# Kernel tuning notes

Hardware: AMD Instinct MI355X
Metric: run time of the kernel (lower is better)

## Reference

```python
import jax, jax.numpy as jnp
import numpy as np

HIDDEN = 1024
HEADS = 16
HEAD_DIM = HIDDEN // HEADS  # 64
B, S = 2, 2048


def setup_inputs() -> dict:
    key = jax.random.key(0)
    ks = jax.random.split(key, 12)
    lim_h = 1.0 / np.sqrt(HEAD_DIM)
    lim_o = 1.0 / np.sqrt(HIDDEN)
    u = lambda k, shape, lim: jax.random.uniform(k, shape, jnp.float32, -lim, lim)
    return {
        "query": jax.random.normal(ks[0], (B, S, HIDDEN), jnp.float32),
        "key": jax.random.normal(ks[1], (B, S, HIDDEN), jnp.float32),
        "value": jax.random.normal(ks[2], (B, S, HIDDEN), jnp.float32),
        "mask": jax.random.randint(ks[3], (B, 1, S, S), 0, 2, jnp.int32),
        "Wq": u(ks[4], (HEAD_DIM, HEAD_DIM), lim_h), "bq": u(ks[5], (HEAD_DIM,), lim_h),
        "Wk": u(ks[6], (HEAD_DIM, HEAD_DIM), lim_h), "bk": u(ks[7], (HEAD_DIM,), lim_h),
        "Wv": u(ks[8], (HEAD_DIM, HEAD_DIM), lim_h), "bv": u(ks[9], (HEAD_DIM,), lim_h),
        "Wo": u(ks[10], (HIDDEN, HIDDEN), lim_o), "bo": u(ks[11], (HIDDEN,), lim_o),
    }


def reference(query, key, value, mask, Wq, bq, Wk, bk, Wv, bv, Wo, bo):
    b = query.shape[0]
    # view [B, S, H, D]; per-head linear is SHARED across heads (head_dim x head_dim)
    q = query.reshape(b, -1, HEADS, HEAD_DIM) @ Wq.T + bq
    k = key.reshape(b, -1, HEADS, HEAD_DIM) @ Wk.T + bk
    v = value.reshape(b, -1, HEADS, HEAD_DIM) @ Wv.T + bv
    scores = jnp.einsum('nqhd,nkhd->nhqk', q, k)  # [B, H, Sq, Sk]
    scores = jnp.where(mask == 0, jnp.float32(-1e20), scores)
    # NOTE: original scales by sqrt(hidden_dim), not sqrt(head_dim)
    attn = jax.nn.softmax(scores / np.sqrt(HIDDEN).astype(np.float32), axis=3)
    out = jnp.einsum('nhql,nlhd->nqhd', attn, v).reshape(b, query.shape[1], HIDDEN)
    return out @ Wo.T + bo
```

## Files before the change

### kernel.cpp

```cpp
#include <hip/hip_runtime.h>
#include <hip/hip_bf16.h>

#define NB 2
#define NS 2048
#define NH 16
#define ND 64
#define NHID 1024

#define QSCALE 0.045084220f

typedef __attribute__((ext_vector_type(8))) short bf16x8;
typedef __attribute__((ext_vector_type(4))) short s16x4;
typedef __attribute__((ext_vector_type(4))) float f32x4;

typedef __attribute__((address_space(3))) unsigned int lds_u32;
typedef __attribute__((address_space(1))) unsigned int glb_u32;

__device__ inline void gl_lds16(const void* g, void* l) {
  __builtin_amdgcn_global_load_lds((const glb_u32*)g, (lds_u32*)l, 16, 0, 0);
}

__device__ inline short f2bf(float f) {
  __hip_bfloat16 h = __float2bfloat16(f);
  short s; __builtin_memcpy(&s, &h, 2); return s;
}

__device__ inline unsigned pk2bf(float a, float b) {
  float2 t; t.x = a; t.y = b;
  __hip_bfloat162 h = __float22bfloat162_rn(t);
  unsigned u; __builtin_memcpy(&u, &h, 4); return u;
}

__device__ inline bf16x8 cvt8(const float* __restrict__ p) {
  float4 x = *(const float4*)p;
  float4 y = *(const float4*)(p + 4);
  bf16x8 r;
  r[0] = f2bf(x.x); r[1] = f2bf(x.y); r[2] = f2bf(x.z); r[3] = f2bf(x.w);
  r[4] = f2bf(y.x); r[5] = f2bf(y.y); r[6] = f2bf(y.z); r[7] = f2bf(y.w);
  return r;
}

__global__ __launch_bounds__(256) void prep(
    const int* __restrict__ mask, unsigned* __restrict__ mp,
    const float* __restrict__ Wq, const float* __restrict__ Wk,
    const float* __restrict__ Wv, const float* __restrict__ Wo,
    short* __restrict__ Wq_b, short* __restrict__ Wk_b,
    short* __restrict__ Wv_b, short* __restrict__ Wo_b)
{
  if (blockIdx.x < 1024) {
    int idx = blockIdx.x * 256 + threadIdx.x;
    const int4* src = (const int4*)(mask + (long)idx * 32);
    unsigned w = 0;
#pragma unroll
    for (int i = 0; i < 8; ++i) {
      int4 v = src[i];
      w |= (v.x != 0 ? 1u : 0u) << (i * 4 + 0);
      w |= (v.y != 0 ? 1u : 0u) << (i * 4 + 1);
      w |= (v.z != 0 ? 1u : 0u) << (i * 4 + 2);
      w |= (v.w != 0 ? 1u : 0u) << (i * 4 + 3);
    }
    mp[idx] = w;
  } else {
    int i = ((blockIdx.x - 1024) * 256 + threadIdx.x) * 4;
    const float* src; short* dst; int off; float sc = 1.0f;
    if (i < 1048576)      { src = Wo; dst = Wo_b; off = i; }
    else {
      int j = i - 1048576;
      if (j < 4096)       { src = Wq; dst = Wq_b; off = j; sc = QSCALE; }
      else if (j < 8192)  { src = Wk; dst = Wk_b; off = j - 4096; }
      else                { src = Wv; dst = Wv_b; off = j - 8192; }
    }
    float4 v = *(const float4*)(src + off);
    s16x4 o;
    o[0] = f2bf(v.x * sc); o[1] = f2bf(v.y * sc);
    o[2] = f2bf(v.z * sc); o[3] = f2bf(v.w * sc);
    *(s16x4*)(dst + off) = o;
  }
}

__global__ __launch_bounds__(256) void qkv_proj(
    const float* __restrict__ qin, const float* __restrict__ kin,
    const float* __restrict__ vin,
    const short* __restrict__ Wq_b, const float* __restrict__ bq,
    const short* __restrict__ Wk_b, const float* __restrict__ bk,
    const short* __restrict__ Wv_b, const float* __restrict__ bv,
    short* __restrict__ Qws, short* __restrict__ Kws, short* __restrict__ Vt)
{
  __shared__ __align__(16) short ldsT[4][16][72];
  __shared__ __align__(16) short ldsVT[64][72];
  const int tid = threadIdx.x;
  const int w = tid >> 6, lane = tid & 63;
  const int c = lane & 15, qq = lane >> 4;

  if (blockIdx.x < 1024) {
    const int t = blockIdx.x * 4 + w;
    const int b = t >> 11, s = t & (NS - 1);
    const int aoff = (t * 16 + c) * 64 + qq * 8;
    const int row0 = lane >> 3, inner = lane & 7;

#pragma unroll
    for (int m = 0; m < 2; ++m) {
      const float* X  = (m == 0) ? qin  : kin;
      const short* W  = (m == 0) ? Wq_b : Wk_b;
      const float* bb = (m == 0) ? bq   : bk;
      short* dst      = (m == 0) ? Qws  : Kws;
      const float bsc = (m == 0) ? QSCALE : 1.0f;

      bf16x8 a0 = cvt8(X + aoff);
      bf16x8 a1 = cvt8(X + aoff + 32);

#pragma unroll
      for (int nt = 0; nt < 4; ++nt) {
        f32x4 z = {0.f, 0.f, 0.f, 0.f};
        const short* wp = W + (nt * 16 + c) * 64 + qq * 8;
        bf16x8 b0 = *(const bf16x8*)(wp);
        bf16x8 b1 = *(const bf16x8*)(wp + 32);
        z = __builtin_amdgcn_mfma_f32_16x16x32_bf16(a0, b0, z, 0, 0, 0);
        z = __builtin_amdgcn_mfma_f32_16x16x32_bf16(a1, b1, z, 0, 0, 0);
        float bias = bb[nt * 16 + c] * bsc;
#pragma unroll
        for (int r = 0; r < 4; ++r)
          ldsT[w][qq * 4 + r][nt * 16 + c] = f2bf(z[r] + bias);
      }

      bf16x8 v0 = *(const bf16x8*)&ldsT[w][row0][inner * 8];
      bf16x8 v1 = *(const bf16x8*)&ldsT[w][row0 + 8][inner * 8];
      int bh0 = b * NH + row0, bh1 = b * NH + row0 + 8;
      *(bf16x8*)(dst + (bh0 * NS + s) * 64 + inner * 8) = v0;
      *(bf16x8*)(dst + (bh1 * NS + s) * 64 + inner * 8) = v1;
    }
  } else {
    const int bid = blockIdx.x - 1024;
    const int g = w;
    const int bh = bid >> 5;
    const int stile = bid & 31;
    const int b = bh >> 4, h = bh & 15;
    const int sb = stile * 64;

    bf16x8 wv[8];
    float bias[4];
#pragma unroll
    for (int nt = 0; nt < 4; ++nt) {
      const short* wp = Wv_b + (nt * 16 + c) * 64 + qq * 8;
      wv[nt * 2]     = *(const bf16x8*)(wp);
      wv[nt * 2 + 1] = *(const bf16x8*)(wp + 32);
      bias[nt] = bv[nt * 16 + c];
    }

    const float* ap = vin + ((size_t)((b * NS + sb + 16 * g + c) * 16 + h)) * 64 + qq * 8;
    bf16x8 a0 = cvt8(ap);
    bf16x8 a1 = cvt8(ap + 32);
#pragma unroll
    for (int nt = 0; nt < 4; ++nt) {
      f32x4 z = {0.f, 0.f, 0.f, 0.f};
      z = __builtin_amdgcn_mfma_f32_16x16x32_bf16(a0, wv[nt * 2], z, 0, 0, 0);
      z = __builtin_amdgcn_mfma_f32_16x16x32_bf16(a1, wv[nt * 2 + 1], z, 0, 0, 0);
      uint2 u;
      u.x = pk2bf(z[0] + bias[nt], z[1] + bias[nt]);
      u.y = pk2bf(z[2] + bias[nt], z[3] + bias[nt]);
      *(uint2*)&ldsVT[nt * 16 + c][16 * g + qq * 4] = u;
    }
    __syncthreads();

#pragma unroll
    for (int j = 0; j < 2; ++j) {
      int idx = tid + 256 * j;
      int d = idx >> 3, unit = idx & 7;
      bf16x8 o = *(const bf16x8*)&ldsVT[d][unit * 8];
      *(bf16x8*)(Vt + ((size_t)(bh * 64 + d)) * NS + sb + unit * 8) = o;
    }
  }
}

__global__ __launch_bounds__(256) void attn(
    const short* __restrict__ Qws, const short* __restrict__ Kws,
    const short* __restrict__ Vt, const unsigned* __restrict__ Mp,
    short* __restrict__ AO)
{
  __shared__ __align__(16) short Ks[2][64][64];
  __shared__ __align__(16) short Vs[2][64][64];
  __shared__ __align__(16) short Ps[4][32][72];

  const int tid = threadIdx.x;
  const int w = tid >> 6, lane = tid & 63;
  const int c = lane & 15, qq = lane >> 4;
  const int bh = blockIdx.x & 31;
  const int qtile = blockIdx.x >> 5;
  const int b = bh >> 4, h = bh & 15;
  const int qbase = qtile * 128 + w * 32;

  const short* Qp = Qws + (size_t)bh * (NS * 64);
  const short* Kp = Kws + (size_t)bh * (NS * 64);
  const short* Vp = Vt + (size_t)bh * (64 * NS);
  const unsigned* mrow = Mp + (size_t)b * (NS * (NS / 32));

  bf16x8 aq[2][2];
#pragma unroll
  for (int nq = 0; nq < 2; ++nq) {
    const short* qp = Qp + (qbase + nq * 16 + c) * 64 + qq * 8;
    aq[nq][0] = *(const bf16x8*)(qp);
    aq[nq][1] = *(const bf16x8*)(qp + 32);
  }

  bf16x8 ones;
#pragma unroll
  for (int i = 0; i < 8; ++i) ones[i] = (short)0x3F80;

  const f32x4 ZV = {0.f, 0.f, 0.f, 0.f};
  f32x4 O[2][4];
  f32x4 Osum[2];
#pragma unroll
  for (int nq = 0; nq < 2; ++nq) {
    Osum[nq] = ZV;
#pragma unroll
    for (int dt = 0; dt < 4; ++dt) O[nq][dt] = ZV;
  }

  const int srow = lane >> 3;
  const int sunit = (lane & 7) ^ srow;
  auto stage = [&](int kt, int buf) {
#pragma unroll
    for (int i = 0; i < 2; ++i) {
      int j = w * 2 + i;
      const short* gk = Kp + ((size_t)(kt * 64 + j * 8 + srow)) * 64 + sunit * 8;
      gl_lds16(gk, &Ks[buf][0][0] + j * 512);
      const short* gv = Vp + ((size_t)(j * 8 + srow)) * NS + kt * 64 + sunit * 8;
      gl_lds16(gv, &Vs[buf][0][0] + j * 512);
    }
  };

  stage(0, 0);
  __syncthreads();

  for (int kt = 0; kt < NS / 64; ++kt) {
    const int buf = kt & 1;
    if (kt < NS / 64 - 1) stage(kt + 1, buf ^ 1);

    uint2 mw[2];
#pragma unroll
    for (int nq = 0; nq < 2; ++nq)
      mw[nq] = *(const uint2*)(mrow +
          (size_t)(qbase + nq * 16 + c) * (NS / 32) + kt * 2);

#pragma unroll
    for (int mt = 0; mt < 4; ++mt) {
      const short* kb = &Ks[buf][mt * 16 + c][0];
      bf16x8 ak0 = *(const bf16x8*)(kb + ((qq ^ (c & 7)) << 3));
      bf16x8 ak1 = *(const bf16x8*)(kb + (((4 + qq) ^ (c & 7)) << 3));
#pragma unroll
      for (int nq = 0; nq < 2; ++nq) {
        f32x4 z = __builtin_amdgcn_mfma_f32_16x16x32_bf16(ak0, aq[nq][0], ZV, 0, 0, 0);
        z = __builtin_amdgcn_mfma_f32_16x16x32_bf16(ak1, aq[nq][1], z, 0, 0, 0);
        unsigned wsel = (mt & 2) ? mw[nq].y : mw[nq].x;
        unsigned nib = (wsel >> (((mt & 1) << 4) + (qq << 2))) & 0xFu;
        float e0 = __builtin_amdgcn_exp2f((nib & 1u) ? z[0] : -128.f);
        float e1 = __builtin_amdgcn_exp2f((nib & 2u) ? z[1] : -128.f);
        float e2 = __builtin_amdgcn_exp2f((nib & 4u) ? z[2] : -128.f);
        float e3 = __builtin_amdgcn_exp2f((nib & 8u) ? z[3] : -128.f);
        uint2 u;
        u.x = pk2bf(e0, e1);
        u.y = pk2bf(e2, e3);
        *(uint2*)&Ps[w][nq * 16 + c][mt * 16 + (qq << 2)] = u;
      }
    }

#pragma unroll
    for (int ks = 0; ks < 2; ++ks) {
      bf16x8 pf[2];
#pragma unroll
      for (int nq = 0; nq < 2; ++nq) {
        pf[nq] = *(const bf16x8*)&Ps[w][nq * 16 + c][ks * 32 + qq * 8];
        Osum[nq] = __builtin_amdgcn_mfma_f32_16x16x32_bf16(ones, pf[nq], Osum[nq], 0, 0, 0);
      }
#pragma unroll
      for (int dt = 0; dt < 4; ++dt) {
        const short* vb = &Vs[buf][dt * 16 + c][0];
        bf16x8 vf = *(const bf16x8*)(vb + ((((ks << 2) + qq) ^ (c & 7)) << 3));
#pragma unroll
        for (int nq = 0; nq < 2; ++nq)
          O[nq][dt] = __builtin_amdgcn_mfma_f32_16x16x32_bf16(vf, pf[nq], O[nq][dt], 0, 0, 0);
      }
    }

    __syncthreads();
  }

#pragma unroll
  for (int nq = 0; nq < 2; ++nq) {
    float inv = 1.0f / fmaxf(Osum[nq][0], 1e-30f);
    int row = qbase + nq * 16 + c;
#pragma unroll
    for (int dt = 0; dt < 4; ++dt) {
      uint2 u;
      u.x = pk2bf(O[nq][dt][0] * inv, O[nq][dt][1] * inv);
      u.y = pk2bf(O[nq][dt][2] * inv, O[nq][dt][3] * inv);
      *(uint2*)(AO + ((size_t)(b * NS + row)) * NHID + h * 64 + dt * 16 + qq * 4) = u;
    }
  }
}

__global__ __launch_bounds__(256, 2) void oproj(
    const short* __restrict__ X, const short* __restrict__ Wo_b,
    const float* __restrict__ bo, float* __restrict__ out)
{
  __shared__ __align__(16) short As[2][64][64];
  __shared__ __align__(16) short Bs[2][128][64];
  const int tid = threadIdx.x;
  const int w = tid >> 6, lane = tid & 63;
  const int c = lane & 15, qq = lane >> 4;
  const int rowbase = blockIdx.x * 64;
  const int colbase = blockIdx.y * 128;
  const int mh = w & 1, nh = w >> 1;

  const int srow = lane >> 3;
  const int sunit = (lane & 7) ^ srow;

  auto stage = [&](int kb, int buf) {
#pragma unroll
    for (int i = 0; i < 6; ++i) {
      int t = w * 6 + i;
      if (t < 8) {
        const short* g = X + (size_t)(rowbase + t * 8 + srow) * NHID
                           + kb * 64 + sunit * 8;
        gl_lds16(g, &As[buf][0][0] + t * 512);
      } else {
        int j = t - 8;
        const short* g = Wo_b + (size_t)(colbase + j * 8 + srow) * NHID
                              + kb * 64 + sunit * 8;
        gl_lds16(g, &Bs[buf][0][0] + j * 512);
      }
    }
  };

  f32x4 acc[2][4];
#pragma unroll
  for (int mt = 0; mt < 2; ++mt)
#pragma unroll
    for (int nt = 0; nt < 4; ++nt) { f32x4 z = {0.f, 0.f, 0.f, 0.f}; acc[mt][nt] = z; }

  stage(0, 0);
  __syncthreads();

  for (int kb = 0; kb < NHID / 64; ++kb) {
    const int buf = kb & 1;
    if (kb < NHID / 64 - 1) stage(kb + 1, buf ^ 1);

    bf16x8 af[2][2];
#pragma unroll
    for (int mt = 0; mt < 2; ++mt) {
      const short* ap = &As[buf][mh * 32 + mt * 16 + c][0];
#pragma unroll
      for (int ks = 0; ks < 2; ++ks)
        af[mt][ks] = *(const bf16x8*)(ap + ((((ks << 2) + qq) ^ (c & 7)) << 3));
    }
#pragma unroll
    for (int nt = 0; nt < 4; ++nt) {
      const short* bp = &Bs[buf][nh * 64 + nt * 16 + c][0];
#pragma unroll
      for (int ks = 0; ks < 2; ++ks) {
        bf16x8 bf = *(const bf16x8*)(bp + ((((ks << 2) + qq) ^ (c & 7)) << 3));
#pragma unroll
        for (int mt = 0; mt < 2; ++mt)
          acc[mt][nt] = __builtin_amdgcn_mfma_f32_16x16x32_bf16(af[mt][ks], bf, acc[mt][nt], 0, 0, 0);
      }
    }

    __syncthreads();
  }

#pragma unroll
  for (int nt = 0; nt < 4; ++nt) {
    int col = colbase + nh * 64 + nt * 16 + c;
    float bias = bo[col];
#pragma unroll
    for (int mt = 0; mt < 2; ++mt) {
      int row = rowbase + mh * 32 + mt * 16 + qq * 4;
#pragma unroll
      for (int r = 0; r < 4; ++r)
        out[(size_t)(row + r) * NHID + col] = acc[mt][nt][r] + bias;
    }
  }
}

extern "C" void kernel_launch(void* const* d_in, const int* in_sizes, int n_in,
                              void* d_out, int out_size, void* d_ws, size_t ws_size,
                              hipStream_t stream) {
  const float* qin = (const float*)d_in[0];
  const float* kin = (const float*)d_in[1];
  const float* vin = (const float*)d_in[2];
  const int*  mask = (const int*)d_in[3];
  const float* Wq = (const float*)d_in[4];
  const float* bq = (const float*)d_in[5];
  const float* Wk = (const float*)d_in[6];
  const float* bk = (const float*)d_in[7];
  const float* Wv = (const float*)d_in[8];
  const float* bv = (const float*)d_in[9];
  const float* Wo = (const float*)d_in[10];
  const float* bo = (const float*)d_in[11];
  float* out = (float*)d_out;

  char* ws = (char*)d_ws;
  short* Qws = (short*)(ws);
  short* Kws = (short*)(ws + (size_t)(8 << 20));
  short* Vt  = (short*)(ws + (size_t)(16 << 20));
  short* AO  = (short*)(ws + (size_t)(24 << 20));
  unsigned* Mp = (unsigned*)(ws + (size_t)(32 << 20));
  short* Wo_b = (short*)(ws + (size_t)(33 << 20));
  short* Wq_b = (short*)(ws + (size_t)(35 << 20));
  short* Wk_b = (short*)(ws + (size_t)(35 << 20) + 8192);
  short* Wv_b = (short*)(ws + (size_t)(35 << 20) + 16384);

  prep<<<2060, 256, 0, stream>>>(mask, Mp, Wq, Wk, Wv, Wo, Wq_b, Wk_b, Wv_b, Wo_b);
  qkv_proj<<<2048, 256, 0, stream>>>(qin, kin, vin, Wq_b, bq, Wk_b, bk, Wv_b, bv,
                                     Qws, Kws, Vt);
  attn<<<(NB * NH) * (NS / 128), 256, 0, stream>>>(Qws, Kws, Vt, Mp, AO);
  oproj<<<dim3(64, 8), 256, 0, stream>>>(AO, Wo_b, bo, out);
}
```

Baseline: 222.5 us.

## Load V fragments directly from global, replace MFMA row-sum with scalar sum

The attention kernel stops staging V tiles through LDS and instead has each lane load its V MFMA fragments straight from global memory into registers at the top of each key tile. The softmax denominator is now accumulated as a per-lane fp32 sum of the exponentials and reduced with cross-lane shuffles at the end, replacing the extra MFMA against a ones vector. Launch bounds now request four blocks per CU. This cuts LDS traffic and footprint and removes MFMA work, but exposes global-load latency for V with only the loop-level prefetch of K overlapping it, and raises register pressure from holding eight V fragments.

```diff
diff --git a/kernel.cpp b/kernel.cpp
--- a/kernel.cpp
+++ b/kernel.cpp
@@ -172,13 +172,12 @@
   }
 }
 
-__global__ __launch_bounds__(256) void attn(
+__global__ __launch_bounds__(256, 4) void attn(
     const short* __restrict__ Qws, const short* __restrict__ Kws,
     const short* __restrict__ Vt, const unsigned* __restrict__ Mp,
     short* __restrict__ AO)
 {
   __shared__ __align__(16) short Ks[2][64][64];
-  __shared__ __align__(16) short Vs[2][64][64];
   __shared__ __align__(16) short Ps[4][32][72];
 
   const int tid = threadIdx.x;
@@ -202,39 +201,41 @@
     aq[nq][1] = *(const bf16x8*)(qp + 32);
   }
 
-  bf16x8 ones;
-#pragma unroll
-  for (int i = 0; i < 8; ++i) ones[i] = (short)0x3F80;
-
   const f32x4 ZV = {0.f, 0.f, 0.f, 0.f};
+  float lsum[2] = {0.f, 0.f};
   f32x4 O[2][4];
-  f32x4 Osum[2];
-#pragma unroll
-  for (int nq = 0; nq < 2; ++nq) {
-    Osum[nq] = ZV;
+#pragma unroll
+  for (int nq = 0; nq < 2; ++nq)
 #pragma unroll
     for (int dt = 0; dt < 4; ++dt) O[nq][dt] = ZV;
-  }
 
   const int srow = lane >> 3;
   const int sunit = (lane & 7) ^ srow;
-  auto stage = [&](int kt, int buf) {
+  auto stageK = [&](int kt, int buf) {
 #pragma unroll
     for (int i = 0; i < 2; ++i) {
       int j = w * 2 + i;
       const short* gk = Kp + ((size_t)(kt * 64 + j * 8 + srow)) * 64 + sunit * 8;
       gl_lds16(gk, &Ks[buf][0][0] + j * 512);
-      const short* gv = Vp + ((size_t)(j * 8 + srow)) * NS + kt * 64 + sunit * 8;
-      gl_lds16(gv, &Vs[buf][0][0] + j * 512);
     }
   };
 
-  stage(0, 0);
+  stageK(0, 0);
   __syncthreads();
 
   for (int kt = 0; kt < NS / 64; ++kt) {
     const int buf = kt & 1;
-    if (kt < NS / 64 - 1) stage(kt + 1, buf ^ 1);
+    const int kbase = kt * 64;
+
+    bf16x8 vf[8];
+#pragma unroll
+    for (int ks = 0; ks < 2; ++ks)
+#pragma unroll
+      for (int dt = 0; dt < 4; ++dt)
+        vf[ks * 4 + dt] = *(const bf16x8*)(Vp +
+            (size_t)(dt * 16 + c) * NS + kbase + ks * 32 + qq * 8);
+
+    if (kt < NS / 64 - 1) stageK(kt + 1, buf ^ 1);
 
     uint2 mw[2];
 #pragma unroll
@@ -257,6 +258,7 @@
         float e1 = __builtin_amdgcn_exp2f((nib & 2u) ? z[1] : -128.f);
         float e2 = __builtin_amdgcn_exp2f((nib & 4u) ? z[2] : -128.f);
         float e3 = __builtin_amdgcn_exp2f((nib & 8u) ? z[3] : -128.f);
+        lsum[nq] += (e0 + e1) + (e2 + e3);
         uint2 u;
         u.x = pk2bf(e0, e1);
         u.y = pk2bf(e2, e3);
@@ -268,18 +270,13 @@
     for (int ks = 0; ks < 2; ++ks) {
       bf16x8 pf[2];
 #pragma unroll
-      for (int nq = 0; nq < 2; ++nq) {
+      for (int nq = 0; nq < 2; ++nq)
         pf[nq] = *(const bf16x8*)&Ps[w][nq * 16 + c][ks * 32 + qq * 8];
-        Osum[nq] = __builtin_amdgcn_mfma_f32_16x16x32_bf16(ones, pf[nq], Osum[nq], 0, 0, 0);
-      }
-#pragma unroll
-      for (int dt = 0; dt < 4; ++dt) {
-        const short* vb = &Vs[buf][dt * 16 + c][0];
-        bf16x8 vf = *(const bf16x8*)(vb + ((((ks << 2) + qq) ^ (c & 7)) << 3));
+#pragma unroll
+      for (int dt = 0; dt < 4; ++dt)
 #pragma unroll
         for (int nq = 0; nq < 2; ++nq)
-          O[nq][dt] = __builtin_amdgcn_mfma_f32_16x16x32_bf16(vf, pf[nq], O[nq][dt], 0, 0, 0);
-      }
+          O[nq][dt] = __builtin_amdgcn_mfma_f32_16x16x32_bf16(vf[ks * 4 + dt], pf[nq], O[nq][dt], 0, 0, 0);
     }
 
     __syncthreads();
@@ -287,13 +284,20 @@
 
 #pragma unroll
   for (int nq = 0; nq < 2; ++nq) {
-    float inv = 1.0f / fmaxf(Osum[nq][0], 1e-30f);
+    float v = lsum[nq];
+    v += __shfl_xor(v, 16);
+    v += __shfl_xor(v, 32);
+    lsum[nq] = 1.0f / fmaxf(v, 1e-30f);
+  }
+
+#pragma unroll
+  for (int nq = 0; nq < 2; ++nq) {
     int row = qbase + nq * 16 + c;
 #pragma unroll
     for (int dt = 0; dt < 4; ++dt) {
       uint2 u;
-      u.x = pk2bf(O[nq][dt][0] * inv, O[nq][dt][1] * inv);
-      u.y = pk2bf(O[nq][dt][2] * inv, O[nq][dt][3] * inv);
+      u.x = pk2bf(O[nq][dt][0] * lsum[nq], O[nq][dt][1] * lsum[nq]);
+      u.y = pk2bf(O[nq][dt][2] * lsum[nq], O[nq][dt][3] * lsum[nq]);
       *(uint2*)(AO + ((size_t)(b * NS + row)) * NHID + h * 64 + dt * 16 + qq * 4) = u;
     }
   }
```

Result: slower. 260.5 us (+17.0%).

## Fuse prep into projection kernel and replace MFMA row-sum with scalar sums

Applied to the files above, without the earlier changes.

Merges the mask-packing and weight-conversion prep kernel into the QKV projection kernel as extra block ranges. The small Wq/Wk/Wv weights are now converted to bf16 on the fly inside each block instead of being staged through workspace. This removes one launch and the dependency between the two kernels, at the cost of redundant per-block weight conversion. In attention, the softmax denominator is now accumulated from the fp32 exponentials with cross-lane shuffles rather than an extra ones-vector MFMA per tile, which cuts matrix-core work and uses unrounded values for the sum.

```diff
diff --git a/kernel.cpp b/kernel.cpp
--- a/kernel.cpp
+++ b/kernel.cpp
@@ -34,57 +34,30 @@
 __device__ inline bf16x8 cvt8(const float* __restrict__ p) {
   float4 x = *(const float4*)p;
   float4 y = *(const float4*)(p + 4);
-  bf16x8 r;
-  r[0] = f2bf(x.x); r[1] = f2bf(x.y); r[2] = f2bf(x.z); r[3] = f2bf(x.w);
-  r[4] = f2bf(y.x); r[5] = f2bf(y.y); r[6] = f2bf(y.z); r[7] = f2bf(y.w);
-  return r;
-}
-
-__global__ __launch_bounds__(256) void prep(
-    const int* __restrict__ mask, unsigned* __restrict__ mp,
-    const float* __restrict__ Wq, const float* __restrict__ Wk,
-    const float* __restrict__ Wv, const float* __restrict__ Wo,
-    short* __restrict__ Wq_b, short* __restrict__ Wk_b,
-    short* __restrict__ Wv_b, short* __restrict__ Wo_b)
-{
-  if (blockIdx.x < 1024) {
-    int idx = blockIdx.x * 256 + threadIdx.x;
-    const int4* src = (const int4*)(mask + (long)idx * 32);
-    unsigned w = 0;
-#pragma unroll
-    for (int i = 0; i < 8; ++i) {
-      int4 v = src[i];
-      w |= (v.x != 0 ? 1u : 0u) << (i * 4 + 0);
-      w |= (v.y != 0 ? 1u : 0u) << (i * 4 + 1);
-      w |= (v.z != 0 ? 1u : 0u) << (i * 4 + 2);
-      w |= (v.w != 0 ? 1u : 0u) << (i * 4 + 3);
-    }
-    mp[idx] = w;
-  } else {
-    int i = ((blockIdx.x - 1024) * 256 + threadIdx.x) * 4;
-    const float* src; short* dst; int off; float sc = 1.0f;
-    if (i < 1048576)      { src = Wo; dst = Wo_b; off = i; }
-    else {
-      int j = i - 1048576;
-      if (j < 4096)       { src = Wq; dst = Wq_b; off = j; sc = QSCALE; }
-      else if (j < 8192)  { src = Wk; dst = Wk_b; off = j - 4096; }
-      else                { src = Wv; dst = Wv_b; off = j - 8192; }
-    }
-    float4 v = *(const float4*)(src + off);
-    s16x4 o;
-    o[0] = f2bf(v.x * sc); o[1] = f2bf(v.y * sc);
-    o[2] = f2bf(v.z * sc); o[3] = f2bf(v.w * sc);
-    *(s16x4*)(dst + off) = o;
-  }
-}
-
-__global__ __launch_bounds__(256) void qkv_proj(
+  unsigned u[4];
+  u[0] = pk2bf(x.x, x.y); u[1] = pk2bf(x.z, x.w);
+  u[2] = pk2bf(y.x, y.y); u[3] = pk2bf(y.z, y.w);
+  bf16x8 r; __builtin_memcpy(&r, u, 16); return r;
+}
+
+__device__ inline bf16x8 cvt8s(const float* __restrict__ p, float sc) {
+  float4 x = *(const float4*)p;
+  float4 y = *(const float4*)(p + 4);
+  unsigned u[4];
+  u[0] = pk2bf(x.x * sc, x.y * sc); u[1] = pk2bf(x.z * sc, x.w * sc);
+  u[2] = pk2bf(y.x * sc, y.y * sc); u[3] = pk2bf(y.z * sc, y.w * sc);
+  bf16x8 r; __builtin_memcpy(&r, u, 16); return r;
+}
+
+__global__ __launch_bounds__(256) void fused_front(
     const float* __restrict__ qin, const float* __restrict__ kin,
-    const float* __restrict__ vin,
-    const short* __restrict__ Wq_b, const float* __restrict__ bq,
-    const short* __restrict__ Wk_b, const float* __restrict__ bk,
-    const short* __restrict__ Wv_b, const float* __restrict__ bv,
-    short* __restrict__ Qws, short* __restrict__ Kws, short* __restrict__ Vt)
+    const float* __restrict__ vin, const int* __restrict__ mask,
+    const float* __restrict__ Wq, const float* __restrict__ bq,
+    const float* __restrict__ Wk, const float* __restrict__ bk,
+    const float* __restrict__ Wv, const float* __restrict__ bv,
+    const float* __restrict__ Wo,
+    short* __restrict__ Qws, short* __restrict__ Kws, short* __restrict__ Vt,
+    unsigned* __restrict__ mp, short* __restrict__ Wo_b)
 {
   __shared__ __align__(16) short ldsT[4][16][72];
   __shared__ __align__(16) short ldsVT[64][72];
@@ -100,24 +73,24 @@
 
 #pragma unroll
     for (int m = 0; m < 2; ++m) {
-      const float* X  = (m == 0) ? qin  : kin;
-      const short* W  = (m == 0) ? Wq_b : Wk_b;
-      const float* bb = (m == 0) ? bq   : bk;
-      short* dst      = (m == 0) ? Qws  : Kws;
-      const float bsc = (m == 0) ? QSCALE : 1.0f;
+      const float* X  = (m == 0) ? qin : kin;
+      const float* Wf = (m == 0) ? Wq  : Wk;
+      const float* bb = (m == 0) ? bq  : bk;
+      short* dst      = (m == 0) ? Qws : Kws;
+      const float sc  = (m == 0) ? QSCALE : 1.0f;
 
       bf16x8 a0 = cvt8(X + aoff);
       bf16x8 a1 = cvt8(X + aoff + 32);
 
 #pragma unroll
       for (int nt = 0; nt < 4; ++nt) {
+        const float* wp = Wf + (nt * 16 + c) * 64 + qq * 8;
+        bf16x8 b0 = cvt8s(wp, sc);
+        bf16x8 b1 = cvt8s(wp + 32, sc);
         f32x4 z = {0.f, 0.f, 0.f, 0.f};
-        const short* wp = W + (nt * 16 + c) * 64 + qq * 8;
-        bf16x8 b0 = *(const bf16x8*)(wp);
-        bf16x8 b1 = *(const bf16x8*)(wp + 32);
         z = __builtin_amdgcn_mfma_f32_16x16x32_bf16(a0, b0, z, 0, 0, 0);
         z = __builtin_amdgcn_mfma_f32_16x16x32_bf16(a1, b1, z, 0, 0, 0);
-        float bias = bb[nt * 16 + c] * bsc;
+        float bias = bb[nt * 16 + c] * sc;
 #pragma unroll
         for (int r = 0; r < 4; ++r)
           ldsT[w][qq * 4 + r][nt * 16 + c] = f2bf(z[r] + bias);
@@ -129,7 +102,7 @@
       *(bf16x8*)(dst + (bh0 * NS + s) * 64 + inner * 8) = v0;
       *(bf16x8*)(dst + (bh1 * NS + s) * 64 + inner * 8) = v1;
     }
-  } else {
+  } else if (blockIdx.x < 2048) {
     const int bid = blockIdx.x - 1024;
     const int g = w;
     const int bh = bid >> 5;
@@ -141,9 +114,9 @@
     float bias[4];
 #pragma unroll
     for (int nt = 0; nt < 4; ++nt) {
-      const short* wp = Wv_b + (nt * 16 + c) * 64 + qq * 8;
-      wv[nt * 2]     = *(const bf16x8*)(wp);
-      wv[nt * 2 + 1] = *(const bf16x8*)(wp + 32);
+      const float* wp = Wv + (nt * 16 + c) * 64 + qq * 8;
+      wv[nt * 2]     = cvt8(wp);
+      wv[nt * 2 + 1] = cvt8(wp + 32);
       bias[nt] = bv[nt * 16 + c];
     }
 
@@ -169,6 +142,26 @@
       bf16x8 o = *(const bf16x8*)&ldsVT[d][unit * 8];
       *(bf16x8*)(Vt + ((size_t)(bh * 64 + d)) * NS + sb + unit * 8) = o;
     }
+  } else if (blockIdx.x < 3072) {
+    int idx = (blockIdx.x - 2048) * 256 + tid;
+    const int4* src = (const int4*)(mask + (long)idx * 32);
+    unsigned wbits = 0;
+#pragma unroll
+    for (int i = 0; i < 8; ++i) {
+      int4 v = src[i];
+      wbits |= (v.x != 0 ? 1u : 0u) << (i * 4 + 0);
+      wbits |= (v.y != 0 ? 1u : 0u) << (i * 4 + 1);
+      wbits |= (v.z != 0 ? 1u : 0u) << (i * 4 + 2);
+      wbits |= (v.w != 0 ? 1u : 0u) << (i * 4 + 3);
+    }
+    mp[idx] = wbits;
+  } else {
+    int i = ((blockIdx.x - 3072) * 256 + tid) * 4;
+    float4 v = *(const float4*)(Wo + i);
+    uint2 o;
+    o.x = pk2bf(v.x, v.y);
+    o.y = pk2bf(v.z, v.w);
+    *(uint2*)(Wo_b + i) = o;
   }
 }
 
@@ -202,19 +195,13 @@
     aq[nq][1] = *(const bf16x8*)(qp + 32);
   }
 
-  bf16x8 ones;
-#pragma unroll
-  for (int i = 0; i < 8; ++i) ones[i] = (short)0x3F80;
-
   const f32x4 ZV = {0.f, 0.f, 0.f, 0.f};
+  float lsum[2] = {0.f, 0.f};
   f32x4 O[2][4];
-  f32x4 Osum[2];
-#pragma unroll
-  for (int nq = 0; nq < 2; ++nq) {
-    Osum[nq] = ZV;
+#pragma unroll
+  for (int nq = 0; nq < 2; ++nq)
 #pragma unroll
     for (int dt = 0; dt < 4; ++dt) O[nq][dt] = ZV;
-  }
 
   const int srow = lane >> 3;
   const int sunit = (lane & 7) ^ srow;
@@ -257,6 +244,7 @@
         float e1 = __builtin_amdgcn_exp2f((nib & 2u) ? z[1] : -128.f);
         float e2 = __builtin_amdgcn_exp2f((nib & 4u) ? z[2] : -128.f);
         float e3 = __builtin_amdgcn_exp2f((nib & 8u) ? z[3] : -128.f);
+        lsum[nq] += (e0 + e1) + (e2 + e3);
         uint2 u;
         u.x = pk2bf(e0, e1);
         u.y = pk2bf(e2, e3);
@@ -268,10 +256,8 @@
     for (int ks = 0; ks < 2; ++ks) {
       bf16x8 pf[2];
 #pragma unroll
-      for (int nq = 0; nq < 2; ++nq) {
+      for (int nq = 0; nq < 2; ++nq)
         pf[nq] = *(const bf16x8*)&Ps[w][nq * 16 + c][ks * 32 + qq * 8];
-        Osum[nq] = __builtin_amdgcn_mfma_f32_16x16x32_bf16(ones, pf[nq], Osum[nq], 0, 0, 0);
-      }
 #pragma unroll
       for (int dt = 0; dt < 4; ++dt) {
         const short* vb = &Vs[buf][dt * 16 + c][0];
@@ -287,13 +273,20 @@
 
 #pragma unroll
   for (int nq = 0; nq < 2; ++nq) {
-    float inv = 1.0f / fmaxf(Osum[nq][0], 1e-30f);
+    float v = lsum[nq];
+    v += __shfl_xor(v, 16);
+    v += __shfl_xor(v, 32);
+    lsum[nq] = 1.0f / fmaxf(v, 1e-30f);
+  }
+
+#pragma unroll
+  for (int nq = 0; nq < 2; ++nq) {
     int row = qbase + nq * 16 + c;
 #pragma unroll
     for (int dt = 0; dt < 4; ++dt) {
       uint2 u;
-      u.x = pk2bf(O[nq][dt][0] * inv, O[nq][dt][1] * inv);
-      u.y = pk2bf(O[nq][dt][2] * inv, O[nq][dt][3] * inv);
+      u.x = pk2bf(O[nq][dt][0] * lsum[nq], O[nq][dt][1] * lsum[nq]);
+      u.y = pk2bf(O[nq][dt][2] * lsum[nq], O[nq][dt][3] * lsum[nq]);
       *(uint2*)(AO + ((size_t)(b * NS + row)) * NHID + h * 64 + dt * 16 + qq * 4) = u;
     }
   }
@@ -406,13 +399,9 @@
   short* AO  = (short*)(ws + (size_t)(24 << 20));
   unsigned* Mp = (unsigned*)(ws + (size_t)(32 << 20));
   short* Wo_b = (short*)(ws + (size_t)(33 << 20));
-  short* Wq_b = (short*)(ws + (size_t)(35 << 20));
-  short* Wk_b = (short*)(ws + (size_t)(35 << 20) + 8192);
-  short* Wv_b = (short*)(ws + (size_t)(35 << 20) + 16384);
-
-  prep<<<2060, 256, 0, stream>>>(mask, Mp, Wq, Wk, Wv, Wo, Wq_b, Wk_b, Wv_b, Wo_b);
-  qkv_proj<<<2048, 256, 0, stream>>>(qin, kin, vin, Wq_b, bq, Wk_b, bk, Wv_b, bv,
-                                     Qws, Kws, Vt);
+
+  fused_front<<<4096, 256, 0, stream>>>(qin, kin, vin, mask, Wq, bq, Wk, bk,
+                                        Wv, bv, Wo, Qws, Kws, Vt, Mp, Wo_b);
   attn<<<(NB * NH) * (NS / 128), 256, 0, stream>>>(Qws, Kws, Vt, Mp, AO);
   oproj<<<dim3(64, 8), 256, 0, stream>>>(AO, Wo_b, bo, out);
 }
```

Result: slower. 232.5 us (+4.5%).
